# Performance work log

Hardware: AMD Instinct MI355X
Metric: run time of the kernel (lower is better)

Reference implementation:

```python
import jax, jax.numpy as jnp
import numpy as np

N, F_IN, F_OUT, H = 4096, 128, 64, 8
NEG_SLOPE = 0.2

def leaky_relu(x):
    return jnp.where(x >= 0, x, NEG_SLOPE * x)

def setup_inputs() -> dict:
    key = jax.random.key(0)
    k = jax.random.split(key, 6)
    x = jax.random.normal(k[0], (N, F_IN), dtype=jnp.float32)
    conn = jax.random.uniform(k[1], (N, N)) < 0.1
    conn = conn | jnp.eye(N, dtype=bool)
    topology = jnp.where(conn, 0.0, -1e9).astype(jnp.float32)
    proj = jax.random.normal(k[2], (H, F_IN, F_OUT), dtype=jnp.float32) * (1.0 / np.sqrt(F_IN))
    score_src = jax.random.normal(k[3], (H, F_OUT), dtype=jnp.float32) * (1.0 / np.sqrt(F_OUT))
    score_dst = jax.random.normal(k[4], (H, F_OUT), dtype=jnp.float32) * (1.0 / np.sqrt(F_OUT))
    skip_w = jax.random.normal(k[5], (H * F_OUT, F_IN), dtype=jnp.float32) * (1.0 / np.sqrt(F_IN))
    return {"x": x, "topology": topology, "proj": proj,
            "score_src": score_src, "score_dst": score_dst, "skip_w": skip_w}

def reference(x, topology, proj, score_src, score_dst, skip_w):
    # dropout is identity at inference time
    # projected node features: [H, N, F_OUT]
    h = jnp.einsum('ni,hio->hno', x, proj)
    # additive attention scores (GAT): [H, N, 1] + [H, 1, N] -> [H, N, N]
    s_src = jnp.einsum('hno,ho->hn', h, score_src)
    s_dst = jnp.einsum('hno,ho->hn', h, score_dst)
    scores = leaky_relu(s_src[:, :, None] + s_dst[:, None, :])
    attn = jax.nn.softmax(scores + topology[None, :, :], axis=-1)  # [H, N, N]
    # aggregate neighbors, then transpose heads to [N, H, F_OUT]
    out = jnp.einsum('hij,hjo->iho', attn, h)
    # skip connection (F_OUT != F_IN -> projected skip)
    out = out + (x @ skip_w.T).reshape(N, H, F_OUT)
    # mean over heads (concat_heads=False), then LeakyReLU activation
    out = leaky_relu(jnp.mean(out, axis=1))  # [N, F_OUT]
    return out
```

## Files before the change

kernel.cpp:

```cpp
#include <hip/hip_runtime.h>
#include <hip/hip_bf16.h>

#define NN 4096
#define FIN 128
#define FOUT 64
#define NH 8
#define KS 4
#define QT 32

typedef float f32x4 __attribute__((ext_vector_type(4)));
typedef __bf16 bf16x8 __attribute__((ext_vector_type(8)));
typedef unsigned long long u64;

__global__ __launch_bounds__(256) void wc_kernel(
    const float* __restrict__ proj, const float* __restrict__ score_src,
    const float* __restrict__ score_dst, const float* __restrict__ skip_w,
    float* __restrict__ Wc) {
    int idx = blockIdx.x * 256 + threadIdx.x;
    if (idx >= FIN * 80) return;
    int i = idx / 80, c = idx % 80;
    float v = 0.f;
    if (c < 16) {
        int h = c & 7;
        const float* w = (c < 8 ? score_src : score_dst) + h * FOUT;
        const float* p = proj + (size_t)h * FIN * FOUT + (size_t)i * FOUT;
        for (int f = 0; f < FOUT; ++f) v += p[f] * w[f];
    } else {
        int f = c - 16;
        for (int h = 0; h < NH; ++h) v += skip_w[(size_t)(h * FOUT + f) * FIN + i];
        v *= 0.125f;
    }
    Wc[i * 80 + c] = v;
}

__global__ __launch_bounds__(256) void scores_kernel(
    const float* __restrict__ x, const float* __restrict__ Wc,
    float* __restrict__ skipm, unsigned* __restrict__ EF, float2* __restrict__ C12,
    __hip_bfloat16* __restrict__ xb_) {
    __shared__ float wcs[FIN][80];
    __shared__ float xs[16][FIN + 5];
    const int n0 = blockIdx.x * 16;
    const int tid = threadIdx.x;
    for (int i = tid; i < FIN * 80 / 4; i += 256)
        ((float4*)&wcs[0][0])[i] = ((const float4*)Wc)[i];
    const float4* xsrc = (const float4*)(x + (size_t)n0 * FIN);
    for (int i = tid; i < 16 * FIN / 4; i += 256) {
        int r = i >> 5, c4 = i & 31;
        *(float4*)&xs[r][c4 * 4] = xsrc[i];
    }
    __syncthreads();
    const int r = tid & 15;
    const int g = tid >> 4;
    float acc[4];
    float sa = 0.f;
#pragma unroll
    for (int j = 0; j < 4; ++j) acc[j] = 0.f;
#pragma unroll 4
    for (int i = 0; i < FIN; ++i) {
        float xv = xs[r][i];
        float4 p = *(float4*)&wcs[i][16 + g * 4];
        float qv = wcs[i][g];
        acc[0] += xv * p.x; acc[1] += xv * p.y; acc[2] += xv * p.z; acc[3] += xv * p.w;
        sa += xv * qv;
    }
    int n = n0 + r;
#pragma unroll
    for (int j = 0; j < 4; ++j) skipm[(size_t)n * FOUT + g * 4 + j] = acc[j];
    if (g < 8) {
        C12[g * NN + n] = make_float2(expf(sa), expf(0.2f * sa));
    } else {
        __hip_bfloat16 e0 = __float2bfloat16(expf(sa));
        __hip_bfloat16 f0 = __float2bfloat16(expf(0.2f * sa));
        EF[(g - 8) * NN + n] = ((unsigned)*(unsigned short*)&f0 << 16) | (unsigned)*(unsigned short*)&e0;
    }
    {
        int row = tid >> 4, col0 = (tid & 15) * 8;
        const float* src = &xs[row][col0];
        bf16x8 b0;
#pragma unroll
        for (int j = 0; j < 8; ++j) b0[j] = (__bf16)src[j];
        *(bf16x8*)((__bf16*)xb_ + (size_t)(n0 + row) * FIN + col0) = b0;
    }
}

__global__ __launch_bounds__(256) void vt_kernel(
    const float* __restrict__ proj, const __hip_bfloat16* __restrict__ xb_,
    __hip_bfloat16* __restrict__ Vt_) {
    __shared__ __bf16 pT[FOUT][FIN + 8];
    const int tid = threadIdx.x;
    const int h = blockIdx.x >> 6;
    const int ng = blockIdx.x & 63;
    const __bf16* xb = (const __bf16*)xb_;
    __bf16* Vt = (__bf16*)Vt_;
    for (int idx = tid; idx < FIN * FOUT; idx += 256) {
        int i = idx >> 6, f = idx & 63;
        pT[f][i] = (__bf16)proj[(size_t)h * FIN * FOUT + idx];
    }
    __syncthreads();
    const int wave = tid >> 6, lane = tid & 63, q = lane >> 4, li = lane & 15;
    const int nb = ng * 64 + wave * 16;
    f32x4 acc[4];
#pragma unroll
    for (int n = 0; n < 4; ++n) acc[n] = (f32x4){0.f, 0.f, 0.f, 0.f};
#pragma unroll
    for (int kt = 0; kt < 4; ++kt) {
        bf16x8 bfrag = *(const bf16x8*)(xb + (size_t)(nb + li) * FIN + kt * 32 + q * 8);
#pragma unroll
        for (int ft = 0; ft < 4; ++ft) {
            bf16x8 afrag = *(const bf16x8*)&pT[ft * 16 + li][kt * 32 + q * 8];
            acc[ft] = __builtin_amdgcn_mfma_f32_16x16x32_bf16(afrag, bfrag, acc[ft], 0, 0, 0);
        }
    }
#pragma unroll
    for (int ft = 0; ft < 4; ++ft)
#pragma unroll
        for (int reg = 0; reg < 4; ++reg)
            Vt[((size_t)h * FOUT + ft * 16 + q * 4 + reg) * NN + nb + li] = (__bf16)acc[ft][reg];
}

__global__ __launch_bounds__(256) void mask_kernel(
    const float* __restrict__ topo, u64* __restrict__ mb) {
    const int w = blockIdx.x * 4 + (threadIdx.x >> 6);
    const int lane = threadIdx.x & 63;
    size_t base = (size_t)w * 32;
#pragma unroll 4
    for (int it = 0; it < 32; ++it) {
        size_t u = base + it;
        float t = topo[u * 64 + lane];
        u64 b = __ballot(t > -0.5e9f);
        if (lane == 0) mb[u] = b;
    }
}

__attribute__((amdgpu_waves_per_eu(4)))
__global__ __launch_bounds__(256) void attn_kernel(
    const u64* __restrict__ maskbits, const __hip_bfloat16* __restrict__ Vt_,
    const unsigned* __restrict__ EFg, const float2* __restrict__ C12g,
    __hip_bfloat16* __restrict__ accP, float* __restrict__ rsP) {
    __shared__ u64 maskS[QT][17];
    __shared__ char vA[4][4096];
    __shared__ char vB[4][4096];
    const int tid = threadIdx.x;
    const int w = tid >> 6;
    const int lane = tid & 63, q = lane >> 4, li = lane & 15;
    const int qt = blockIdx.x >> 3, ks = (blockIdx.x >> 1) & 3, hb = blockIdx.x & 1;
    const int h = hb * 4 + w;
    const int row0 = qt * QT;
    const int kb0 = ks * 1024;

    const int r_ = lane >> 2;
    const int sg = ((lane & 3) - (r_ >> 1)) & 3;
    const size_t laneoff = (size_t)r_ * NN + sg * 8;
    const int rdoff = li * 64 + ((q + (li >> 1)) & 3) * 16;

    const __bf16* vb = (const __bf16*)Vt_ + (size_t)h * (FOUT * NN) + kb0;
    const unsigned* efb = EFg + (size_t)h * NN + kb0;

#define DMA_TILE(DST, KT) do {                                                     \
    _Pragma("unroll")                                                              \
    for (int c = 0; c < 4; ++c) {                                                  \
        const __bf16* g_ = vb + (size_t)c * (16 * NN) + (KT) * 32 + laneoff;       \
        __builtin_amdgcn_global_load_lds(                                          \
            (const __attribute__((address_space(1))) void*)g_,                     \
            (__attribute__((address_space(3))) void*)&DST[w][c * 1024], 16, 0, 0); \
    }                                                                              \
} while (0)

    DMA_TILE(vA, 0);
    {
        int i0 = tid, i1 = tid + 256;
        maskS[i0 >> 4][i0 & 15] = maskbits[(size_t)(row0 + (i0 >> 4)) * 64 + ks * 16 + (i0 & 15)];
        maskS[i1 >> 4][i1 & 15] = maskbits[(size_t)(row0 + (i1 >> 4)) * 64 + ks * 16 + (i1 & 15)];
    }
    __syncthreads();

    float C1[2], C2[2];
#pragma unroll
    for (int rt = 0; rt < 2; ++rt) {
        float2 c = C12g[(size_t)h * NN + row0 + rt * 16 + li];
        C1[rt] = c.x; C2[rt] = c.y;
    }
    bf16x8 ones;
#pragma unroll
    for (int j = 0; j < 8; ++j) ones[j] = (__bf16)1.0f;

    f32x4 acc[2][4];
    f32x4 rsacc[2];
#pragma unroll
    for (int rt = 0; rt < 2; ++rt) {
#pragma unroll
        for (int n = 0; n < 4; ++n) acc[rt][n] = (f32x4){0.f, 0.f, 0.f, 0.f};
        rsacc[rt] = (f32x4){0.f, 0.f, 0.f, 0.f};
    }

#define CHUNK_BODY(SRC, DSTN, KT) do {                                                        \
    const unsigned* ep_ = efb + (KT) * 32 + q * 8;                                            \
    uint4 ea_ = *(const uint4*)ep_;                                                           \
    uint4 eb_ = *(const uint4*)(ep_ + 4);                                                     \
    asm volatile("" ::: "memory");                           \
    DMA_TILE(DSTN, ((KT) + 1) & 31);                                                          \
    asm volatile("s_waitcnt vmcnt(4)" ::: "memory");                                          \
    bf16x8 vf_[4];                                                                            \
    _Pragma("unroll")                                                                         \
    for (int n = 0; n < 4; ++n)                                                               \
        vf_[n] = *(const bf16x8*)&SRC[w][n * 1024 + rdoff];                                   \
    unsigned ew_[8] = {ea_.x, ea_.y, ea_.z, ea_.w, eb_.x, eb_.y, eb_.z, eb_.w};               \
    _Pragma("unroll")                                                                         \
    for (int rt = 0; rt < 2; ++rt) {                                                          \
        u64 mw_ = maskS[rt * 16 + li][(KT) >> 1];                                             \
        unsigned mm_ = (unsigned)(mw_ >> (((KT) & 1) * 32 + q * 8)) & 0xffu;                  \
        bf16x8 pf_;                                                                           \
        _Pragma("unroll")                                                                     \
        for (int j = 0; j < 8; ++j) {                                                         \
            unsigned e_ = ew_[j];                                                             \
            float E_ = __uint_as_float(e_ << 16);                                             \
            float F_ = __uint_as_float(e_ & 0xffff0000u);                                     \
            float pv_ = fmaxf(C1[rt] * E_, C2[rt] * F_);                                      \
            pv_ = ((mm_ >> j) & 1u) ? pv_ : 0.f;                                              \
            pf_[j] = (__bf16)pv_;                                                             \
        }                                                                                     \
        rsacc[rt] = __builtin_amdgcn_mfma_f32_16x16x32_bf16(pf_, ones, rsacc[rt], 0, 0, 0);   \
        _Pragma("unroll")                                                                     \
        for (int n = 0; n < 4; ++n)                                                           \
            acc[rt][n] = __builtin_amdgcn_mfma_f32_16x16x32_bf16(pf_, vf_[n], acc[rt][n],     \
                                                                 0, 0, 0);                    \
    }                                                                                         \
} while (0)

#pragma unroll 1
    for (int kt = 0; kt < 32; kt += 2) {
        CHUNK_BODY(vA, vB, kt);
        CHUNK_BODY(vB, vA, kt + 1);
    }
#undef CHUNK_BODY
#undef DMA_TILE

#pragma unroll
    for (int rt = 0; rt < 2; ++rt) {
        if (li == 0) {
#pragma unroll
            for (int reg = 0; reg < 4; ++reg)
                rsP[(size_t)(ks * NH + h) * NN + row0 + rt * 16 + q * 4 + reg] = rsacc[rt][reg];
        }
        __hip_bfloat16* ap = accP + ((size_t)(ks * NH + h) * NN + row0 + rt * 16) * 64;
#pragma unroll
        for (int n = 0; n < 4; ++n)
#pragma unroll
            for (int reg = 0; reg < 4; ++reg)
                ap[(q * 4 + reg) * 64 + n * 16 + li] = __float2bfloat16(acc[rt][n][reg]);
    }
}

__global__ __launch_bounds__(256) void combine_kernel(
    const __hip_bfloat16* __restrict__ accP, const float* __restrict__ rsP,
    float* __restrict__ out) {
    int idx = blockIdx.x * 256 + threadIdx.x;
    int row = idx >> 6, f = idx & 63;
    float s = 0.f;
#pragma unroll 1
    for (int h = 0; h < NH; ++h) {
        float a = 0.f, r = 0.f;
#pragma unroll
        for (int k = 0; k < KS; ++k) {
            a += __bfloat162float(accP[((size_t)(k * NH + h) * NN + row) * 64 + f]);
            r += rsP[(size_t)(k * NH + h) * NN + row];
        }
        s += a / r;
    }
    float v = s * 0.125f + out[idx];
    out[idx] = fmaxf(v, 0.2f * v);
}

extern "C" void kernel_launch(void* const* d_in, const int* in_sizes, int n_in,
                              void* d_out, int out_size, void* d_ws, size_t ws_size,
                              hipStream_t stream) {
    (void)in_sizes; (void)n_in; (void)out_size; (void)ws_size;
    const float* x         = (const float*)d_in[0];
    const float* topology  = (const float*)d_in[1];
    const float* proj      = (const float*)d_in[2];
    const float* score_src = (const float*)d_in[3];
    const float* score_dst = (const float*)d_in[4];
    const float* skip_w    = (const float*)d_in[5];
    float* out = (float*)d_out;

    char* ws = (char*)d_ws;
    __hip_bfloat16* xb = (__hip_bfloat16*)ws;
    __hip_bfloat16* Vt = (__hip_bfloat16*)(ws + 1048576);
    unsigned* EF  = (unsigned*)(ws + 5242880);
    float2* C12   = (float2*)(ws + 5373952);
    float* Wc     = (float*)(ws + 5636096);
    u64* maskbits = (u64*)(ws + 5677056);
    float* rsP    = (float*)(ws + 7774208);
    __hip_bfloat16* accP = (__hip_bfloat16*)(ws + 8298496);
    float* skipm = out;

    wc_kernel<<<40, 256, 0, stream>>>(proj, score_src, score_dst, skip_w, Wc);
    scores_kernel<<<256, 256, 0, stream>>>(x, Wc, skipm, EF, C12, xb);
    vt_kernel<<<512, 256, 0, stream>>>(proj, xb, Vt);
    mask_kernel<<<2048, 256, 0, stream>>>(topology, maskbits);
    attn_kernel<<<1024, 256, 0, stream>>>(maskbits, Vt, EF, C12, accP, rsP);
    combine_kernel<<<1024, 256, 0, stream>>>(accP, rsP, out);
}
```

Before: 187.7 us.

## Fuse weight prep, scores, V projection and mask packing into one prep kernel

```diff
diff --git a/kernel.cpp b/kernel.cpp
--- a/kernel.cpp
+++ b/kernel.cpp
@@ -12,123 +12,135 @@
 typedef __bf16 bf16x8 __attribute__((ext_vector_type(8)));
 typedef unsigned long long u64;
 
-__global__ __launch_bounds__(256) void wc_kernel(
+__global__ __launch_bounds__(256) void prep_kernel(
+    const float* __restrict__ x, const float* __restrict__ topo,
     const float* __restrict__ proj, const float* __restrict__ score_src,
     const float* __restrict__ score_dst, const float* __restrict__ skip_w,
-    float* __restrict__ Wc) {
-    int idx = blockIdx.x * 256 + threadIdx.x;
-    if (idx >= FIN * 80) return;
-    int i = idx / 80, c = idx % 80;
-    float v = 0.f;
-    if (c < 16) {
-        int h = c & 7;
-        const float* w = (c < 8 ? score_src : score_dst) + h * FOUT;
-        const float* p = proj + (size_t)h * FIN * FOUT + (size_t)i * FOUT;
-        for (int f = 0; f < FOUT; ++f) v += p[f] * w[f];
-    } else {
-        int f = c - 16;
-        for (int h = 0; h < NH; ++h) v += skip_w[(size_t)(h * FOUT + f) * FIN + i];
-        v *= 0.125f;
-    }
-    Wc[i * 80 + c] = v;
-}
-
-__global__ __launch_bounds__(256) void scores_kernel(
-    const float* __restrict__ x, const float* __restrict__ Wc,
     float* __restrict__ skipm, unsigned* __restrict__ EF, float2* __restrict__ C12,
-    __hip_bfloat16* __restrict__ xb_) {
-    __shared__ float wcs[FIN][80];
-    __shared__ float xs[16][FIN + 5];
-    const int n0 = blockIdx.x * 16;
+    __hip_bfloat16* __restrict__ Vt_, u64* __restrict__ mb) {
     const int tid = threadIdx.x;
-    for (int i = tid; i < FIN * 80 / 4; i += 256)
-        ((float4*)&wcs[0][0])[i] = ((const float4*)Wc)[i];
+
+    if (blockIdx.x >= 128) {
+        const int w = (blockIdx.x - 128) * 4 + (tid >> 6);
+        const int lane = tid & 63;
+        size_t base = (size_t)w * 32;
+#pragma unroll 4
+        for (int it = 0; it < 32; ++it) {
+            size_t u = base + it;
+            float t = topo[u * 64 + lane];
+            u64 b = __ballot(t > -0.5e9f);
+            if (lane == 0) mb[u] = b;
+        }
+        return;
+    }
+
+    __shared__ float xs[32][FIN + 5];
+    __shared__ __align__(16) char ubuf[40960];
+    float* wcs = (float*)ubuf;
+    const int n0 = blockIdx.x * 32;
+
     const float4* xsrc = (const float4*)(x + (size_t)n0 * FIN);
-    for (int i = tid; i < 16 * FIN / 4; i += 256) {
+    for (int i = tid; i < 32 * FIN / 4; i += 256) {
         int r = i >> 5, c4 = i & 31;
         *(float4*)&xs[r][c4 * 4] = xsrc[i];
     }
+    for (int t = tid; t < 2048; t += 256) {
+        int i = t >> 4, c = t & 15, h = c & 7;
+        const float* wv = (c < 8 ? score_src : score_dst) + h * FOUT;
+        const float* p = proj + (size_t)h * FIN * FOUT + (size_t)i * FOUT;
+        float v = 0.f;
+#pragma unroll 8
+        for (int f = 0; f < FOUT; ++f) v += p[f] * wv[f];
+        wcs[i * 80 + c] = v;
+    }
+    for (int t = tid; t < 8192; t += 256) {
+        int i = t >> 6, f = t & 63;
+        float v = 0.f;
+#pragma unroll
+        for (int h = 0; h < NH; ++h) v += skip_w[(size_t)(h * FOUT + f) * FIN + i];
+        wcs[i * 80 + 16 + f] = 0.125f * v;
+    }
     __syncthreads();
-    const int r = tid & 15;
-    const int g = tid >> 4;
-    float acc[4];
-    float sa = 0.f;
-#pragma unroll
-    for (int j = 0; j < 4; ++j) acc[j] = 0.f;
+
+    {
+        const int r = tid & 31, g = tid >> 5;
+        float acc[8];
+        float sa0 = 0.f, sa1 = 0.f;
+#pragma unroll
+        for (int j = 0; j < 8; ++j) acc[j] = 0.f;
 #pragma unroll 4
-    for (int i = 0; i < FIN; ++i) {
-        float xv = xs[r][i];
-        float4 p = *(float4*)&wcs[i][16 + g * 4];
-        float qv = wcs[i][g];
-        acc[0] += xv * p.x; acc[1] += xv * p.y; acc[2] += xv * p.z; acc[3] += xv * p.w;
-        sa += xv * qv;
-    }
-    int n = n0 + r;
-#pragma unroll
-    for (int j = 0; j < 4; ++j) skipm[(size_t)n * FOUT + g * 4 + j] = acc[j];
-    if (g < 8) {
-        C12[g * NN + n] = make_float2(expf(sa), expf(0.2f * sa));
-    } else {
-        __hip_bfloat16 e0 = __float2bfloat16(expf(sa));
-        __hip_bfloat16 f0 = __float2bfloat16(expf(0.2f * sa));
-        EF[(g - 8) * NN + n] = ((unsigned)*(unsigned short*)&f0 << 16) | (unsigned)*(unsigned short*)&e0;
-    }
+        for (int i = 0; i < FIN; ++i) {
+            float xv = xs[r][i];
+            const float* wr = &wcs[i * 80];
+            float4 p0 = *(float4*)(wr + 16 + g * 8);
+            float4 p1 = *(float4*)(wr + 16 + g * 8 + 4);
+            float2 q0 = *(float2*)(wr + g * 2);
+            acc[0] += xv * p0.x; acc[1] += xv * p0.y; acc[2] += xv * p0.z; acc[3] += xv * p0.w;
+            acc[4] += xv * p1.x; acc[5] += xv * p1.y; acc[6] += xv * p1.z; acc[7] += xv * p1.w;
+            sa0 += xv * q0.x; sa1 += xv * q0.y;
+        }
+        int n = n0 + r;
+#pragma unroll
+        for (int j = 0; j < 8; ++j) skipm[(size_t)n * FOUT + g * 8 + j] = acc[j];
+        int c0 = g * 2;
+        if (c0 < 8) {
+            C12[c0 * NN + n] = make_float2(expf(sa0), expf(0.2f * sa0));
+            C12[(c0 + 1) * NN + n] = make_float2(expf(sa1), expf(0.2f * sa1));
+        } else {
+            __hip_bfloat16 e0 = __float2bfloat16(expf(sa0));
+            __hip_bfloat16 f0 = __float2bfloat16(expf(0.2f * sa0));
+            __hip_bfloat16 e1 = __float2bfloat16(expf(sa1));
+            __hip_bfloat16 f1 = __float2bfloat16(expf(0.2f * sa1));
+            EF[(c0 - 8) * NN + n] = ((unsigned)*(unsigned short*)&f0 << 16) | (unsigned)*(unsigned short*)&e0;
+            EF[(c0 - 7) * NN + n] = ((unsigned)*(unsigned short*)&f1 << 16) | (unsigned)*(unsigned short*)&e1;
+        }
+    }
+    __syncthreads();
+
+    __bf16 (*xbs)[136] = (__bf16 (*)[136])ubuf;
+    __bf16 (*pTs)[136] = (__bf16 (*)[136])(ubuf + 8704);
     {
-        int row = tid >> 4, col0 = (tid & 15) * 8;
+        int row = tid >> 3, col0 = (tid & 7) * 16;
         const float* src = &xs[row][col0];
-        bf16x8 b0;
-#pragma unroll
-        for (int j = 0; j < 8; ++j) b0[j] = (__bf16)src[j];
-        *(bf16x8*)((__bf16*)xb_ + (size_t)(n0 + row) * FIN + col0) = b0;
-    }
-}
-
-__global__ __launch_bounds__(256) void vt_kernel(
-    const float* __restrict__ proj, const __hip_bfloat16* __restrict__ xb_,
-    __hip_bfloat16* __restrict__ Vt_) {
-    __shared__ __bf16 pT[FOUT][FIN + 8];
-    const int tid = threadIdx.x;
-    const int h = blockIdx.x >> 6;
-    const int ng = blockIdx.x & 63;
-    const __bf16* xb = (const __bf16*)xb_;
-    __bf16* Vt = (__bf16*)Vt_;
+        bf16x8 b0, b1;
+#pragma unroll
+        for (int j = 0; j < 8; ++j) { b0[j] = (__bf16)src[j]; b1[j] = (__bf16)src[8 + j]; }
+        *(bf16x8*)&xbs[row][col0] = b0;
+        *(bf16x8*)&xbs[row][col0 + 8] = b1;
+    }
     for (int idx = tid; idx < FIN * FOUT; idx += 256) {
         int i = idx >> 6, f = idx & 63;
-        pT[f][i] = (__bf16)proj[(size_t)h * FIN * FOUT + idx];
+        pTs[f][i] = (__bf16)proj[idx];
     }
     __syncthreads();
-    const int wave = tid >> 6, lane = tid & 63, q = lane >> 4, li = lane & 15;
-    const int nb = ng * 64 + wave * 16;
-    f32x4 acc[4];
-#pragma unroll
-    for (int n = 0; n < 4; ++n) acc[n] = (f32x4){0.f, 0.f, 0.f, 0.f};
-#pragma unroll
-    for (int kt = 0; kt < 4; ++kt) {
-        bf16x8 bfrag = *(const bf16x8*)(xb + (size_t)(nb + li) * FIN + kt * 32 + q * 8);
-#pragma unroll
-        for (int ft = 0; ft < 4; ++ft) {
-            bf16x8 afrag = *(const bf16x8*)&pT[ft * 16 + li][kt * 32 + q * 8];
-            acc[ft] = __builtin_amdgcn_mfma_f32_16x16x32_bf16(afrag, bfrag, acc[ft], 0, 0, 0);
-        }
-    }
-#pragma unroll
-    for (int ft = 0; ft < 4; ++ft)
-#pragma unroll
-        for (int reg = 0; reg < 4; ++reg)
-            Vt[((size_t)h * FOUT + ft * 16 + q * 4 + reg) * NN + nb + li] = (__bf16)acc[ft][reg];
-}
-
-__global__ __launch_bounds__(256) void mask_kernel(
-    const float* __restrict__ topo, u64* __restrict__ mb) {
-    const int w = blockIdx.x * 4 + (threadIdx.x >> 6);
-    const int lane = threadIdx.x & 63;
-    size_t base = (size_t)w * 32;
-#pragma unroll 4
-    for (int it = 0; it < 32; ++it) {
-        size_t u = base + it;
-        float t = topo[u * 64 + lane];
-        u64 b = __ballot(t > -0.5e9f);
-        if (lane == 0) mb[u] = b;
+
+    const int lane = tid & 63, q = lane >> 4, li = lane & 15, w = tid >> 6;
+    __bf16* Vt = (__bf16*)Vt_;
+#pragma unroll 1
+    for (int h = 0; h < NH; ++h) {
+#pragma unroll
+        for (int rt = 0; rt < 2; ++rt) {
+            f32x4 va = (f32x4){0.f, 0.f, 0.f, 0.f};
+#pragma unroll
+            for (int kt = 0; kt < 4; ++kt) {
+                bf16x8 bfrag = *(const bf16x8*)&xbs[rt * 16 + li][kt * 32 + q * 8];
+                bf16x8 afrag = *(const bf16x8*)&pTs[w * 16 + li][kt * 32 + q * 8];
+                va = __builtin_amdgcn_mfma_f32_16x16x32_bf16(afrag, bfrag, va, 0, 0, 0);
+            }
+#pragma unroll
+            for (int reg = 0; reg < 4; ++reg)
+                Vt[((size_t)h * FOUT + w * 16 + q * 4 + reg) * NN + n0 + rt * 16 + li] =
+                    (__bf16)va[reg];
+        }
+        __syncthreads();
+        if (h < 7) {
+            const float* ph = proj + (size_t)(h + 1) * FIN * FOUT;
+            for (int idx = tid; idx < FIN * FOUT; idx += 256) {
+                int i = idx >> 6, f = idx & 63;
+                pTs[f][i] = (__bf16)ph[idx];
+            }
+            __syncthreads();
+        }
     }
 }
 
@@ -284,20 +296,16 @@
     float* out = (float*)d_out;
 
     char* ws = (char*)d_ws;
-    __hip_bfloat16* xb = (__hip_bfloat16*)ws;
     __hip_bfloat16* Vt = (__hip_bfloat16*)(ws + 1048576);
     unsigned* EF  = (unsigned*)(ws + 5242880);
     float2* C12   = (float2*)(ws + 5373952);
-    float* Wc     = (float*)(ws + 5636096);
     u64* maskbits = (u64*)(ws + 5677056);
     float* rsP    = (float*)(ws + 7774208);
     __hip_bfloat16* accP = (__hip_bfloat16*)(ws + 8298496);
     float* skipm = out;
 
-    wc_kernel<<<40, 256, 0, stream>>>(proj, score_src, score_dst, skip_w, Wc);
-    scores_kernel<<<256, 256, 0, stream>>>(x, Wc, skipm, EF, C12, xb);
-    vt_kernel<<<512, 256, 0, stream>>>(proj, xb, Vt);
-    mask_kernel<<<2048, 256, 0, stream>>>(topology, maskbits);
+    prep_kernel<<<2176, 256, 0, stream>>>(x, topology, proj, score_src, score_dst,
+                                          skip_w, skipm, EF, C12, Vt, maskbits);
     attn_kernel<<<1024, 256, 0, stream>>>(maskbits, Vt, EF, C12, accP, rsP);
     combine_kernel<<<1024, 256, 0, stream>>>(accP, rsP, out);
 }
```

After: 226.6 us. +20.8%, slower.
